# Kernel optimization log

Measured on AMD Instinct MI355X. Metric: run time of the kernel, lower is better.

Reference implementation:

```python
import jax, jax.numpy as jnp
import numpy as np

N_NODES = 100000


def _graph_conv(x, W, b, src, dst, n_nodes):
    # DGL GraphConv, norm='both', weight applied before aggregation (in>out).
    E = src.shape[0]
    ones = jnp.ones((E,), dtype=x.dtype)
    out_deg = jax.ops.segment_sum(ones, src, num_segments=n_nodes)
    in_deg = jax.ops.segment_sum(ones, dst, num_segments=n_nodes)
    out_norm = jnp.clip(out_deg, 1.0, None) ** -0.5  # [N]
    in_norm = jnp.clip(in_deg, 1.0, None) ** -0.5    # [N]
    h = (x * out_norm[:, None]) @ W                  # [N, out] dense GEMM first
    msg = h[src]                                     # gather  [E, out]
    agg = jax.ops.segment_sum(msg, dst, num_segments=n_nodes)  # scatter-add
    return agg * in_norm[:, None] + b


def setup_inputs() -> dict:
    key = jax.random.key(0)
    k1, k2, k3, k4, k5 = jax.random.split(key, 5)
    E = 1600000
    features = jax.random.normal(k1, (N_NODES, 128), dtype=jnp.float32)
    src = jax.random.randint(k2, (E,), 0, N_NODES, dtype=jnp.int64)
    dst = jax.random.randint(k3, (E,), 0, N_NODES, dtype=jnp.int64)
    W1 = jax.random.normal(k4, (128, 64), dtype=jnp.float32) * (1.0 / np.sqrt(128))
    b1 = jnp.zeros((64,), dtype=jnp.float32)
    W2 = jax.random.normal(k5, (64, 32), dtype=jnp.float32) * (1.0 / np.sqrt(64))
    b2 = jnp.zeros((32,), dtype=jnp.float32)
    return {"features": features, "src": src, "dst": dst,
            "W1": W1, "b1": b1, "W2": W2, "b2": b2}


def reference(features, src, dst, W1, b1, W2, b2):
    x = jax.nn.relu(_graph_conv(features, W1, b1, src, dst, N_NODES))
    x = _graph_conv(x, W2, b2, src, dst, N_NODES)
    return x
```

## Files before the change

### kernel.cpp

```cpp
#include <hip/hip_runtime.h>
#include <hip/hip_bf16.h>


#define BSH 7
#define BNODES 128
#define SRCMASK 0x1FFFF
#define CAP 2560
#define CHUNK 4096

typedef __attribute__((ext_vector_type(8))) short bf16x8;
typedef __attribute__((ext_vector_type(4))) float f32x4;

__device__ __forceinline__ unsigned short f2bf(float f) {
    unsigned int u = __float_as_uint(f);
    return (unsigned short)((u + 0x7FFFu + ((u >> 16) & 1u)) >> 16);
}

__device__ __forceinline__ float bflo(unsigned int u) {
    return __uint_as_float(u << 16);
}
__device__ __forceinline__ float bfhi(unsigned int u) {
    return __uint_as_float(u & 0xFFFF0000u);
}

__global__ __launch_bounds__(1024) void k_place(const int* __restrict__ src,
        const int* __restrict__ dst, int* __restrict__ ebuf,
        unsigned char* __restrict__ sbuf, int* __restrict__ offs,
        int* __restrict__ soffs, int E) {
    __shared__ int lh[800], s[800];
    int t = threadIdx.x;
    int e0 = blockIdx.x * CHUNK;
    int nE = min(CHUNK, E - e0);
    int sv[4], dv[4];
#pragma unroll
    for (int j = 0; j < 4; j++) {
        int i = t + 1024 * j;
        if (i < nE) { sv[j] = src[e0 + i]; dv[j] = dst[e0 + i]; }
        else        { sv[j] = -1; }
    }
    if (t < 800) lh[t] = 0;
    __syncthreads();
#pragma unroll
    for (int j = 0; j < 4; j++) if (sv[j] >= 0) {
        atomicAdd(&lh[dv[j] >> BSH], 0x10000);
        atomicAdd(&lh[sv[j] >> BSH], 1);
    }
    __syncthreads();
    if (t < 800) s[t] = lh[t];
    __syncthreads();
    for (int o = 1; o < 800; o <<= 1) {
        int u = (t < 800 && t >= o) ? s[t - o] : 0;
        __syncthreads();
        if (t < 800) s[t] += u;
        __syncthreads();
    }
    int obase = blockIdx.x * 801;
    if (t < 800) {
        int incl = s[t], c = lh[t];
        int bd = (incl >> 16) - (c >> 16);
        int bs = (incl & 0xFFFF) - (c & 0xFFFF);
        offs[obase + t] = bd;
        soffs[obase + t] = bs;
        s[t] = (bd << 16) | bs;
    }
    if (t == 0) { offs[obase + 800] = nE; soffs[obase + 800] = nE; }
    __syncthreads();
#pragma unroll
    for (int j = 0; j < 4; j++) if (sv[j] >= 0) {
        int pd = atomicAdd(&s[dv[j] >> BSH], 0x10000) >> 16;
        ebuf[e0 + pd] = sv[j] | ((dv[j] & (BNODES - 1)) << 17);
        int ps = atomicAdd(&s[sv[j] >> BSH], 1) & 0xFFFF;
        sbuf[e0 + ps] = (unsigned char)(sv[j] & (BNODES - 1));
    }
}

__global__ __launch_bounds__(1024) void k_sg1(const int* __restrict__ ebuf,
        const unsigned char* __restrict__ sbuf, const int* __restrict__ offs,
        const int* __restrict__ soffs, int* __restrict__ csrc,
        int* __restrict__ ostart, int* __restrict__ oend,
        float* __restrict__ nI, float* __restrict__ nO,
        const float* __restrict__ x, const float* __restrict__ W1,
        unsigned short* __restrict__ h1, int n, int NBLK) {
    __shared__ int cnt2[264], scnt2[264], cur2[264];
    __shared__ int cnt[BNODES], s[BNODES];
    __shared__ int segst[400], segen[400], sst[400], sen[400];
    __shared__ float snO[BNODES];
    __shared__ __align__(16) unsigned short sX[128 * 136];
    __shared__ __align__(16) unsigned short sWT[64 * 136];
    int t = threadIdx.x, b = blockIdx.x;

    if (t < NBLK) {
        segst[t] = t * CHUNK + offs[t * 801 + b];
        segen[t] = t * CHUNK + offs[t * 801 + b + 1];
        sst[t]   = t * CHUNK + soffs[t * 801 + b];
        sen[t]   = t * CHUNK + soffs[t * 801 + b + 1];
    }
    if (t < 264) { cnt2[t] = 0; scnt2[t] = 0; }
    __syncthreads();
    int grp = t >> 3, ln = t & 7;
    int hb = (t >> 9) * 132;
    for (int sg = grp; sg < NBLK; sg += 128) {
        int en = segen[sg];
        for (int i = segst[sg] + ln; i < en; i += 8)
            atomicAdd(&cnt2[hb + (ebuf[i] >> 17)], 1);
        int en2 = sen[sg];
        for (int i = sst[sg] + ln; i < en2; i += 8)
            atomicAdd(&scnt2[hb + sbuf[i]], 1);
    }
    __syncthreads();
    if (t < BNODES) {
        cnt[t] = cnt2[t] + cnt2[132 + t];
        s[t] = cnt[t];
    }
    __syncthreads();
    for (int o = 1; o < BNODES; o <<= 1) {
        int u = (t < BNODES && t >= o) ? s[t - o] : 0;
        __syncthreads();
        if (t < BNODES) s[t] += u;
        __syncthreads();
    }
    if (t < BNODES) {
        int e0 = b * CAP;
        int st = e0 + s[t] - cnt[t];
        cur2[t] = st;
        cur2[132 + t] = st + cnt2[t];
        int sct = scnt2[t] + scnt2[132 + t];
        float nov = rsqrtf(fmaxf((float)sct, 1.0f));
        snO[t] = nov;
        int g = b * BNODES + t;
        if (g < n) {
            ostart[g] = st;
            oend[g] = e0 + s[t];
            nI[g] = rsqrtf(fmaxf((float)cnt[t], 1.0f));
            nO[g] = nov;
        }
    }
    __syncthreads();
    for (int sg = grp; sg < NBLK; sg += 128) {
        int en = segen[sg];
        for (int i = segst[sg] + ln; i < en; i += 8) {
            int p = ebuf[i];
            int pos = atomicAdd(&cur2[hb + (p >> 17)], 1);
            csrc[pos] = p & SRCMASK;
        }
    }

    __syncthreads();
    {
        const float4* W4 = (const float4*)W1;
#pragma unroll
        for (int i = 0; i < 2; i++) {
            int f = t + 1024 * i;
            int k = f >> 4, n4 = (f & 15) * 4;
            float4 v = W4[f];
            sWT[(n4 + 0) * 136 + k] = f2bf(v.x);
            sWT[(n4 + 1) * 136 + k] = f2bf(v.y);
            sWT[(n4 + 2) * 136 + k] = f2bf(v.z);
            sWT[(n4 + 3) * 136 + k] = f2bf(v.w);
        }
    }
    const int rowbase = b * BNODES;
    {
        const float4* x4 = (const float4*)x;
#pragma unroll
        for (int i = 0; i < 4; i++) {
            int f = t + 1024 * i;
            int row = f >> 5, kc = f & 31;
            int grow = rowbase + row;
            float4 v = make_float4(0.f, 0.f, 0.f, 0.f);
            float sc = 0.f;
            if (grow < n) { v = x4[(size_t)grow * 32 + kc]; sc = snO[row]; }
            ushort4 o;
            o.x = f2bf(v.x * sc); o.y = f2bf(v.y * sc);
            o.z = f2bf(v.z * sc); o.w = f2bf(v.w * sc);
            *(ushort4*)&sX[row * 136 + kc * 4] = o;
        }
    }
    __syncthreads();
    const int wv = t >> 6, lane = t & 63;
    const int lr = lane & 15, lk = lane >> 4;
    const int slab = (wv & 7) * 16;
    const int ch = (wv >> 3) * 32;
    f32x4 acc0 = {0.f, 0.f, 0.f, 0.f};
    f32x4 acc1 = {0.f, 0.f, 0.f, 0.f};
#pragma unroll
    for (int kk = 0; kk < 4; kk++) {
        bf16x8 a  = *(const bf16x8*)&sX[(slab + lr) * 136 + kk * 32 + lk * 8];
        bf16x8 b0 = *(const bf16x8*)&sWT[(ch + lr) * 136 + kk * 32 + lk * 8];
        bf16x8 b1 = *(const bf16x8*)&sWT[(ch + 16 + lr) * 136 + kk * 32 + lk * 8];
        acc0 = __builtin_amdgcn_mfma_f32_16x16x32_bf16(a, b0, acc0, 0, 0, 0);
        acc1 = __builtin_amdgcn_mfma_f32_16x16x32_bf16(a, b1, acc1, 0, 0, 0);
    }
#pragma unroll
    for (int i = 0; i < 4; i++) {
        int grow = rowbase + slab + lk * 4 + i;
        if (grow < n) {
            size_t base = (size_t)grow * 64 + ch + lr;
            h1[base]      = f2bf(acc0[i]);
            h1[base + 16] = f2bf(acc1[i]);
        }
    }
}

__global__ void k_agg64(const unsigned short* __restrict__ h,
                        const int* __restrict__ csrc,
                        const int* __restrict__ ostart, const int* __restrict__ oend,
                        const float* __restrict__ nI, const float* __restrict__ b1,
                        float* __restrict__ x2, int n) {
    int node = blockIdx.x * 4 + (threadIdx.x >> 6);
    int lane = threadIdx.x & 63;
    if (node >= n) return;
    int s0 = ostart[node], s1 = oend[node];
    int sub = lane >> 3;
    int c8 = (lane & 7) * 8;
    float a[8] = {}, d[8] = {};
    int e = s0;
    for (; e + 15 < s1; e += 16) {
        int p0 = csrc[e + sub];
        int p1 = csrc[e + 8 + sub];
        uint4 u0 = *(const uint4*)&h[(size_t)p0 * 64 + c8];
        uint4 u1 = *(const uint4*)&h[(size_t)p1 * 64 + c8];
        a[0] += bflo(u0.x); a[1] += bfhi(u0.x);
        a[2] += bflo(u0.y); a[3] += bfhi(u0.y);
        a[4] += bflo(u0.z); a[5] += bfhi(u0.z);
        a[6] += bflo(u0.w); a[7] += bfhi(u0.w);
        d[0] += bflo(u1.x); d[1] += bfhi(u1.x);
        d[2] += bflo(u1.y); d[3] += bfhi(u1.y);
        d[4] += bflo(u1.z); d[5] += bfhi(u1.z);
        d[6] += bflo(u1.w); d[7] += bfhi(u1.w);
    }
    for (; e < s1; e += 8) {
        if (e + sub < s1) {
            int p = csrc[e + sub];
            uint4 u = *(const uint4*)&h[(size_t)p * 64 + c8];
            a[0] += bflo(u.x); a[1] += bfhi(u.x);
            a[2] += bflo(u.y); a[3] += bfhi(u.y);
            a[4] += bflo(u.z); a[5] += bfhi(u.z);
            a[6] += bflo(u.w); a[7] += bfhi(u.w);
        }
    }
#pragma unroll
    for (int i = 0; i < 8; i++) a[i] += d[i];
#pragma unroll
    for (int i = 0; i < 8; i++) {
        a[i] += __shfl(a[i], lane ^ 8, 64);
        a[i] += __shfl(a[i], lane ^ 16, 64);
        a[i] += __shfl(a[i], lane ^ 32, 64);
    }
    if (sub == 0) {
        float ni = nI[node];
        float4 o0, o1;
        o0.x = fmaxf(fmaf(a[0], ni, b1[c8 + 0]), 0.f);
        o0.y = fmaxf(fmaf(a[1], ni, b1[c8 + 1]), 0.f);
        o0.z = fmaxf(fmaf(a[2], ni, b1[c8 + 2]), 0.f);
        o0.w = fmaxf(fmaf(a[3], ni, b1[c8 + 3]), 0.f);
        o1.x = fmaxf(fmaf(a[4], ni, b1[c8 + 4]), 0.f);
        o1.y = fmaxf(fmaf(a[5], ni, b1[c8 + 5]), 0.f);
        o1.z = fmaxf(fmaf(a[6], ni, b1[c8 + 6]), 0.f);
        o1.w = fmaxf(fmaf(a[7], ni, b1[c8 + 7]), 0.f);
        *(float4*)&x2[(size_t)node * 64 + c8] = o0;
        *(float4*)&x2[(size_t)node * 64 + c8 + 4] = o1;
    }
}

__global__ __launch_bounds__(256) void k_gemm2(const float* __restrict__ x2,
                        const float* __restrict__ W2, const float* __restrict__ nO,
                        unsigned short* __restrict__ h2, int n) {
    __shared__ __align__(16) unsigned short sX[128 * 72];
    __shared__ __align__(16) unsigned short sWT[32 * 72];
    const int t = threadIdx.x;
    {
        const float4* W4 = (const float4*)W2;
#pragma unroll
        for (int i = 0; i < 2; i++) {
            int f = t + 256 * i;
            int k = f >> 3, n4 = (f & 7) * 4;
            float4 v = W4[f];
            sWT[(n4 + 0) * 72 + k] = f2bf(v.x);
            sWT[(n4 + 1) * 72 + k] = f2bf(v.y);
            sWT[(n4 + 2) * 72 + k] = f2bf(v.z);
            sWT[(n4 + 3) * 72 + k] = f2bf(v.w);
        }
    }
    const int rowbase = blockIdx.x * 128;
    {
        const float4* x4 = (const float4*)x2;
#pragma unroll
        for (int i = 0; i < 8; i++) {
            int f = t + 256 * i;
            int row = f >> 4, kc = f & 15;
            int grow = rowbase + row;
            float4 v = make_float4(0.f, 0.f, 0.f, 0.f);
            float sc = 0.f;
            if (grow < n) { v = x4[(size_t)grow * 16 + kc]; sc = nO[grow]; }
            ushort4 o;
            o.x = f2bf(v.x * sc); o.y = f2bf(v.y * sc);
            o.z = f2bf(v.z * sc); o.w = f2bf(v.w * sc);
            *(ushort4*)&sX[row * 72 + kc * 4] = o;
        }
    }
    __syncthreads();
    const int wv = t >> 6, lane = t & 63;
    const int lr = lane & 15, lk = lane >> 4;
    const int slab = wv * 32;
    f32x4 a00 = {0.f, 0.f, 0.f, 0.f};
    f32x4 a01 = {0.f, 0.f, 0.f, 0.f};
    f32x4 a10 = {0.f, 0.f, 0.f, 0.f};
    f32x4 a11 = {0.f, 0.f, 0.f, 0.f};
#pragma unroll
    for (int kk = 0; kk < 2; kk++) {
        bf16x8 a0 = *(const bf16x8*)&sX[(slab + lr) * 72 + kk * 32 + lk * 8];
        bf16x8 a1 = *(const bf16x8*)&sX[(slab + 16 + lr) * 72 + kk * 32 + lk * 8];
        bf16x8 b0 = *(const bf16x8*)&sWT[lr * 72 + kk * 32 + lk * 8];
        bf16x8 b1 = *(const bf16x8*)&sWT[(16 + lr) * 72 + kk * 32 + lk * 8];
        a00 = __builtin_amdgcn_mfma_f32_16x16x32_bf16(a0, b0, a00, 0, 0, 0);
        a01 = __builtin_amdgcn_mfma_f32_16x16x32_bf16(a0, b1, a01, 0, 0, 0);
        a10 = __builtin_amdgcn_mfma_f32_16x16x32_bf16(a1, b0, a10, 0, 0, 0);
        a11 = __builtin_amdgcn_mfma_f32_16x16x32_bf16(a1, b1, a11, 0, 0, 0);
    }
#pragma unroll
    for (int i = 0; i < 4; i++) {
        int g0 = rowbase + slab + lk * 4 + i;
        if (g0 < n) {
            h2[(size_t)g0 * 32 + lr]      = f2bf(a00[i]);
            h2[(size_t)g0 * 32 + 16 + lr] = f2bf(a01[i]);
        }
        int g1 = g0 + 16;
        if (g1 < n) {
            h2[(size_t)g1 * 32 + lr]      = f2bf(a10[i]);
            h2[(size_t)g1 * 32 + 16 + lr] = f2bf(a11[i]);
        }
    }
}

__global__ void k_agg32(const unsigned short* __restrict__ h,
                        const int* __restrict__ csrc,
                        const int* __restrict__ ostart, const int* __restrict__ oend,
                        const float* __restrict__ nI, const float* __restrict__ b2,
                        float* __restrict__ out, int n) {
    int node = blockIdx.x * 4 + (threadIdx.x >> 6);
    int lane = threadIdx.x & 63;
    if (node >= n) return;
    int s0 = ostart[node], s1 = oend[node];
    int sub = lane >> 2;
    int c8 = (lane & 3) * 8;
    float a[8] = {};
    int e = s0;
    for (; e + 15 < s1; e += 16) {
        int p = csrc[e + sub];
        uint4 u = *(const uint4*)&h[(size_t)p * 32 + c8];
        a[0] += bflo(u.x); a[1] += bfhi(u.x);
        a[2] += bflo(u.y); a[3] += bfhi(u.y);
        a[4] += bflo(u.z); a[5] += bfhi(u.z);
        a[6] += bflo(u.w); a[7] += bfhi(u.w);
    }
    for (; e < s1; e += 16) {
        if (e + sub < s1) {
            int p = csrc[e + sub];
            uint4 u = *(const uint4*)&h[(size_t)p * 32 + c8];
            a[0] += bflo(u.x); a[1] += bfhi(u.x);
            a[2] += bflo(u.y); a[3] += bfhi(u.y);
            a[4] += bflo(u.z); a[5] += bfhi(u.z);
            a[6] += bflo(u.w); a[7] += bfhi(u.w);
        }
    }
#pragma unroll
    for (int i = 0; i < 8; i++) {
        a[i] += __shfl(a[i], lane ^ 4, 64);
        a[i] += __shfl(a[i], lane ^ 8, 64);
        a[i] += __shfl(a[i], lane ^ 16, 64);
        a[i] += __shfl(a[i], lane ^ 32, 64);
    }
    if (sub == 0) {
        float ni = nI[node];
        float4 o0, o1;
        o0.x = fmaf(a[0], ni, b2[c8 + 0]);
        o0.y = fmaf(a[1], ni, b2[c8 + 1]);
        o0.z = fmaf(a[2], ni, b2[c8 + 2]);
        o0.w = fmaf(a[3], ni, b2[c8 + 3]);
        o1.x = fmaf(a[4], ni, b2[c8 + 4]);
        o1.y = fmaf(a[5], ni, b2[c8 + 5]);
        o1.z = fmaf(a[6], ni, b2[c8 + 6]);
        o1.w = fmaf(a[7], ni, b2[c8 + 7]);
        *(float4*)&out[(size_t)node * 32 + c8] = o0;
        *(float4*)&out[(size_t)node * 32 + c8 + 4] = o1;
    }
}

extern "C" void kernel_launch(void* const* d_in, const int* in_sizes, int n_in,
                              void* d_out, int out_size, void* d_ws, size_t ws_size,
                              hipStream_t stream) {
    const float* x   = (const float*)d_in[0];
    const int*   src = (const int*)d_in[1];
    const int*   dst = (const int*)d_in[2];
    const float* W1  = (const float*)d_in[3];
    const float* b1  = (const float*)d_in[4];
    const float* W2  = (const float*)d_in[5];
    const float* b2  = (const float*)d_in[6];
    float* out = (float*)d_out;

    const int N = in_sizes[0] / 128;
    const int E = in_sizes[1];
    const int NB = (N + BNODES - 1) / BNODES;
    const int NBLK = (E + CHUNK - 1) / CHUNK;

    char* wsb = (char*)d_ws;
    float* nO     = (float*)wsb;  wsb += (size_t)N * 4;
    float* nI     = (float*)wsb;  wsb += (size_t)N * 4;
    int*   ostart = (int*)wsb;    wsb += (size_t)N * 4;
    int*   oend   = (int*)wsb;    wsb += (size_t)N * 4;
    int*   csrc   = (int*)wsb;    wsb += (size_t)NB * CAP * 4;
    int*   offs   = (int*)wsb;    wsb += (size_t)NBLK * 801 * 4;
    unsigned short* h1 = (unsigned short*)wsb;
                                  wsb += (size_t)N * 64 * 2;
    float* x2     = (float*)wsb;  wsb += (size_t)N * 64 * 4;
    unsigned short* h2 = h1;
    int*   ebuf   = (int*)x2;
    unsigned char* sbuf = (unsigned char*)(ebuf) + (size_t)E * 4;
    int*   soffs  = (int*)(sbuf + (size_t)E);

    k_place<<<NBLK, 1024, 0, stream>>>(src, dst, ebuf, sbuf, offs, soffs, E);
    k_sg1<<<NB, 1024, 0, stream>>>(ebuf, sbuf, offs, soffs, csrc,
                                   ostart, oend, nI, nO, x, W1, h1, N, NBLK);

    k_agg64<<<(N + 3) / 4, 256, 0, stream>>>(h1, csrc, ostart, oend, nI, b1, x2, N);

    k_gemm2<<<(N + 127) / 128, 256, 0, stream>>>(x2, W2, nO, h2, N);
    k_agg32<<<(N + 3) / 4, 256, 0, stream>>>(h2, csrc, ostart, oend, nI, b2, out, N);
}
```

Baseline: 249.4 us.

## Fuse layer-1 aggregation with layer-2 GEMM through shared memory

Merges the 64-wide aggregation kernel and the second dense GEMM into one kernel. Each 1024-thread block aggregates 32 nodes, applies bias, ReLU and out-norm, stages the bf16 rows in LDS, then runs MFMA against W2 to write h2. This removes the fp32 x2 round trip through global memory and one launch. In exchange every block reloads and transposes W2, and 12 of 16 waves sit idle during the GEMM phase. The workspace is remapped so h2 aliases the edge scratch buffers.

After: 248.3 us. About the same (-0.5%).

```diff
diff --git a/kernel.cpp b/kernel.cpp
--- a/kernel.cpp
+++ b/kernel.cpp
@@ -202,133 +202,110 @@
     }
 }
 
-__global__ void k_agg64(const unsigned short* __restrict__ h,
-                        const int* __restrict__ csrc,
-                        const int* __restrict__ ostart, const int* __restrict__ oend,
-                        const float* __restrict__ nI, const float* __restrict__ b1,
-                        float* __restrict__ x2, int n) {
-    int node = blockIdx.x * 4 + (threadIdx.x >> 6);
-    int lane = threadIdx.x & 63;
-    if (node >= n) return;
-    int s0 = ostart[node], s1 = oend[node];
-    int sub = lane >> 3;
-    int c8 = (lane & 7) * 8;
-    float a[8] = {}, d[8] = {};
-    int e = s0;
-    for (; e + 15 < s1; e += 16) {
-        int p0 = csrc[e + sub];
-        int p1 = csrc[e + 8 + sub];
-        uint4 u0 = *(const uint4*)&h[(size_t)p0 * 64 + c8];
-        uint4 u1 = *(const uint4*)&h[(size_t)p1 * 64 + c8];
-        a[0] += bflo(u0.x); a[1] += bfhi(u0.x);
-        a[2] += bflo(u0.y); a[3] += bfhi(u0.y);
-        a[4] += bflo(u0.z); a[5] += bfhi(u0.z);
-        a[6] += bflo(u0.w); a[7] += bfhi(u0.w);
-        d[0] += bflo(u1.x); d[1] += bfhi(u1.x);
-        d[2] += bflo(u1.y); d[3] += bfhi(u1.y);
-        d[4] += bflo(u1.z); d[5] += bfhi(u1.z);
-        d[6] += bflo(u1.w); d[7] += bfhi(u1.w);
-    }
-    for (; e < s1; e += 8) {
-        if (e + sub < s1) {
-            int p = csrc[e + sub];
-            uint4 u = *(const uint4*)&h[(size_t)p * 64 + c8];
-            a[0] += bflo(u.x); a[1] += bfhi(u.x);
-            a[2] += bflo(u.y); a[3] += bfhi(u.y);
-            a[4] += bflo(u.z); a[5] += bfhi(u.z);
-            a[6] += bflo(u.w); a[7] += bfhi(u.w);
-        }
-    }
-#pragma unroll
-    for (int i = 0; i < 8; i++) a[i] += d[i];
-#pragma unroll
-    for (int i = 0; i < 8; i++) {
-        a[i] += __shfl(a[i], lane ^ 8, 64);
-        a[i] += __shfl(a[i], lane ^ 16, 64);
-        a[i] += __shfl(a[i], lane ^ 32, 64);
-    }
-    if (sub == 0) {
-        float ni = nI[node];
-        float4 o0, o1;
-        o0.x = fmaxf(fmaf(a[0], ni, b1[c8 + 0]), 0.f);
-        o0.y = fmaxf(fmaf(a[1], ni, b1[c8 + 1]), 0.f);
-        o0.z = fmaxf(fmaf(a[2], ni, b1[c8 + 2]), 0.f);
-        o0.w = fmaxf(fmaf(a[3], ni, b1[c8 + 3]), 0.f);
-        o1.x = fmaxf(fmaf(a[4], ni, b1[c8 + 4]), 0.f);
-        o1.y = fmaxf(fmaf(a[5], ni, b1[c8 + 5]), 0.f);
-        o1.z = fmaxf(fmaf(a[6], ni, b1[c8 + 6]), 0.f);
-        o1.w = fmaxf(fmaf(a[7], ni, b1[c8 + 7]), 0.f);
-        *(float4*)&x2[(size_t)node * 64 + c8] = o0;
-        *(float4*)&x2[(size_t)node * 64 + c8 + 4] = o1;
-    }
-}
-
-__global__ __launch_bounds__(256) void k_gemm2(const float* __restrict__ x2,
-                        const float* __restrict__ W2, const float* __restrict__ nO,
-                        unsigned short* __restrict__ h2, int n) {
-    __shared__ __align__(16) unsigned short sX[128 * 72];
+__global__ __launch_bounds__(1024) void k_ag2(const unsigned short* __restrict__ h,
+        const int* __restrict__ csrc,
+        const int* __restrict__ ostart, const int* __restrict__ oend,
+        const float* __restrict__ nI, const float* __restrict__ nO,
+        const float* __restrict__ b1, const float* __restrict__ W2,
+        unsigned short* __restrict__ h2, int n) {
+    __shared__ __align__(16) unsigned short xt[32 * 72];
     __shared__ __align__(16) unsigned short sWT[32 * 72];
     const int t = threadIdx.x;
+    if (t < 512) {
+        const float4* W4 = (const float4*)W2;
+        int k = t >> 3, n4 = (t & 7) * 4;
+        float4 v = W4[t];
+        sWT[(n4 + 0) * 72 + k] = f2bf(v.x);
+        sWT[(n4 + 1) * 72 + k] = f2bf(v.y);
+        sWT[(n4 + 2) * 72 + k] = f2bf(v.z);
+        sWT[(n4 + 3) * 72 + k] = f2bf(v.w);
+    }
     {
-        const float4* W4 = (const float4*)W2;
-#pragma unroll
-        for (int i = 0; i < 2; i++) {
-            int f = t + 256 * i;
-            int k = f >> 3, n4 = (f & 7) * 4;
-            float4 v = W4[f];
-            sWT[(n4 + 0) * 72 + k] = f2bf(v.x);
-            sWT[(n4 + 1) * 72 + k] = f2bf(v.y);
-            sWT[(n4 + 2) * 72 + k] = f2bf(v.z);
-            sWT[(n4 + 3) * 72 + k] = f2bf(v.w);
-        }
-    }
-    const int rowbase = blockIdx.x * 128;
-    {
-        const float4* x4 = (const float4*)x2;
-#pragma unroll
-        for (int i = 0; i < 8; i++) {
-            int f = t + 256 * i;
-            int row = f >> 4, kc = f & 15;
-            int grow = rowbase + row;
-            float4 v = make_float4(0.f, 0.f, 0.f, 0.f);
-            float sc = 0.f;
-            if (grow < n) { v = x4[(size_t)grow * 16 + kc]; sc = nO[grow]; }
-            ushort4 o;
-            o.x = f2bf(v.x * sc); o.y = f2bf(v.y * sc);
-            o.z = f2bf(v.z * sc); o.w = f2bf(v.w * sc);
-            *(ushort4*)&sX[row * 72 + kc * 4] = o;
-        }
-    }
-    __syncthreads();
-    const int wv = t >> 6, lane = t & 63;
-    const int lr = lane & 15, lk = lane >> 4;
-    const int slab = wv * 32;
-    f32x4 a00 = {0.f, 0.f, 0.f, 0.f};
-    f32x4 a01 = {0.f, 0.f, 0.f, 0.f};
-    f32x4 a10 = {0.f, 0.f, 0.f, 0.f};
-    f32x4 a11 = {0.f, 0.f, 0.f, 0.f};
-#pragma unroll
-    for (int kk = 0; kk < 2; kk++) {
-        bf16x8 a0 = *(const bf16x8*)&sX[(slab + lr) * 72 + kk * 32 + lk * 8];
-        bf16x8 a1 = *(const bf16x8*)&sX[(slab + 16 + lr) * 72 + kk * 32 + lk * 8];
-        bf16x8 b0 = *(const bf16x8*)&sWT[lr * 72 + kk * 32 + lk * 8];
-        bf16x8 b1 = *(const bf16x8*)&sWT[(16 + lr) * 72 + kk * 32 + lk * 8];
-        a00 = __builtin_amdgcn_mfma_f32_16x16x32_bf16(a0, b0, a00, 0, 0, 0);
-        a01 = __builtin_amdgcn_mfma_f32_16x16x32_bf16(a0, b1, a01, 0, 0, 0);
-        a10 = __builtin_amdgcn_mfma_f32_16x16x32_bf16(a1, b0, a10, 0, 0, 0);
-        a11 = __builtin_amdgcn_mfma_f32_16x16x32_bf16(a1, b1, a11, 0, 0, 0);
-    }
-#pragma unroll
-    for (int i = 0; i < 4; i++) {
-        int g0 = rowbase + slab + lk * 4 + i;
-        if (g0 < n) {
-            h2[(size_t)g0 * 32 + lr]      = f2bf(a00[i]);
-            h2[(size_t)g0 * 32 + 16 + lr] = f2bf(a01[i]);
-        }
-        int g1 = g0 + 16;
-        if (g1 < n) {
-            h2[(size_t)g1 * 32 + lr]      = f2bf(a10[i]);
-            h2[(size_t)g1 * 32 + 16 + lr] = f2bf(a11[i]);
+        int* z = (int*)xt;
+        if (t < 32 * 36) z[t] = 0;
+    }
+    __syncthreads();
+    const int wid = t >> 6, lane = t & 63;
+    const int node0 = blockIdx.x * 32;
+    const int sub = lane >> 3;
+    const int c8 = (lane & 7) * 8;
+#pragma unroll
+    for (int g = 0; g < 2; g++) {
+        int node = node0 + wid * 2 + g;
+        if (node < n) {
+            int s0 = ostart[node], s1 = oend[node];
+            float a[8] = {}, d[8] = {};
+            int e = s0;
+            for (; e + 15 < s1; e += 16) {
+                int p0 = csrc[e + sub];
+                int p1 = csrc[e + 8 + sub];
+                uint4 u0 = *(const uint4*)&h[(size_t)p0 * 64 + c8];
+                uint4 u1 = *(const uint4*)&h[(size_t)p1 * 64 + c8];
+                a[0] += bflo(u0.x); a[1] += bfhi(u0.x);
+                a[2] += bflo(u0.y); a[3] += bfhi(u0.y);
+                a[4] += bflo(u0.z); a[5] += bfhi(u0.z);
+                a[6] += bflo(u0.w); a[7] += bfhi(u0.w);
+                d[0] += bflo(u1.x); d[1] += bfhi(u1.x);
+                d[2] += bflo(u1.y); d[3] += bfhi(u1.y);
+                d[4] += bflo(u1.z); d[5] += bfhi(u1.z);
+                d[6] += bflo(u1.w); d[7] += bfhi(u1.w);
+            }
+            for (; e < s1; e += 8) {
+                if (e + sub < s1) {
+                    int p = csrc[e + sub];
+                    uint4 u = *(const uint4*)&h[(size_t)p * 64 + c8];
+                    a[0] += bflo(u.x); a[1] += bfhi(u.x);
+                    a[2] += bflo(u.y); a[3] += bfhi(u.y);
+                    a[4] += bflo(u.z); a[5] += bfhi(u.z);
+                    a[6] += bflo(u.w); a[7] += bfhi(u.w);
+                }
+            }
+#pragma unroll
+            for (int i = 0; i < 8; i++) a[i] += d[i];
+#pragma unroll
+            for (int i = 0; i < 8; i++) {
+                a[i] += __shfl(a[i], lane ^ 8, 64);
+                a[i] += __shfl(a[i], lane ^ 16, 64);
+                a[i] += __shfl(a[i], lane ^ 32, 64);
+            }
+            if (sub == 0) {
+                float ni = nI[node];
+                float nv = nO[node];
+                float v0 = fmaxf(fmaf(a[0], ni, b1[c8 + 0]), 0.f) * nv;
+                float v1 = fmaxf(fmaf(a[1], ni, b1[c8 + 1]), 0.f) * nv;
+                float v2 = fmaxf(fmaf(a[2], ni, b1[c8 + 2]), 0.f) * nv;
+                float v3 = fmaxf(fmaf(a[3], ni, b1[c8 + 3]), 0.f) * nv;
+                float v4 = fmaxf(fmaf(a[4], ni, b1[c8 + 4]), 0.f) * nv;
+                float v5 = fmaxf(fmaf(a[5], ni, b1[c8 + 5]), 0.f) * nv;
+                float v6 = fmaxf(fmaf(a[6], ni, b1[c8 + 6]), 0.f) * nv;
+                float v7 = fmaxf(fmaf(a[7], ni, b1[c8 + 7]), 0.f) * nv;
+                int row = wid * 2 + g;
+                ushort4 o0, o1;
+                o0.x = f2bf(v0); o0.y = f2bf(v1);
+                o0.z = f2bf(v2); o0.w = f2bf(v3);
+                o1.x = f2bf(v4); o1.y = f2bf(v5);
+                o1.z = f2bf(v6); o1.w = f2bf(v7);
+                *(ushort4*)&xt[row * 72 + c8]     = o0;
+                *(ushort4*)&xt[row * 72 + c8 + 4] = o1;
+            }
+        }
+    }
+    __syncthreads();
+    if (wid < 4) {
+        const int lr = lane & 15, lk = lane >> 4;
+        const int slab = wid >> 1, ct = wid & 1;
+        f32x4 acc = {0.f, 0.f, 0.f, 0.f};
+#pragma unroll
+        for (int kk = 0; kk < 2; kk++) {
+            bf16x8 a = *(const bf16x8*)&xt[(slab * 16 + lr) * 72 + kk * 32 + lk * 8];
+            bf16x8 b = *(const bf16x8*)&sWT[(ct * 16 + lr) * 72 + kk * 32 + lk * 8];
+            acc = __builtin_amdgcn_mfma_f32_16x16x32_bf16(a, b, acc, 0, 0, 0);
+        }
+#pragma unroll
+        for (int i = 0; i < 4; i++) {
+            int grow = node0 + slab * 16 + lk * 4 + i;
+            if (grow < n)
+                h2[(size_t)grow * 32 + ct * 16 + lr] = f2bf(acc[i]);
         }
     }
 }
@@ -413,18 +390,18 @@
     int*   offs   = (int*)wsb;    wsb += (size_t)NBLK * 801 * 4;
     unsigned short* h1 = (unsigned short*)wsb;
                                   wsb += (size_t)N * 64 * 2;
-    float* x2     = (float*)wsb;  wsb += (size_t)N * 64 * 4;
-    unsigned short* h2 = h1;
-    int*   ebuf   = (int*)x2;
-    unsigned char* sbuf = (unsigned char*)(ebuf) + (size_t)E * 4;
-    int*   soffs  = (int*)(sbuf + (size_t)E);
+    char*  scr    = wsb;          wsb += (size_t)E * 4 + E + (size_t)NBLK * 801 * 4;
+    int*   ebuf   = (int*)scr;
+    unsigned char* sbuf = (unsigned char*)scr + (size_t)E * 4;
+    int*   soffs  = (int*)((char*)scr + (size_t)E * 4 + E);
+    unsigned short* h2 = (unsigned short*)scr;
 
     k_place<<<NBLK, 1024, 0, stream>>>(src, dst, ebuf, sbuf, offs, soffs, E);
     k_sg1<<<NB, 1024, 0, stream>>>(ebuf, sbuf, offs, soffs, csrc,
                                    ostart, oend, nI, nO, x, W1, h1, N, NBLK);
 
-    k_agg64<<<(N + 3) / 4, 256, 0, stream>>>(h1, csrc, ostart, oend, nI, b1, x2, N);
-
-    k_gemm2<<<(N + 127) / 128, 256, 0, stream>>>(x2, W2, nO, h2, N);
+    k_ag2<<<(N + 31) / 32, 1024, 0, stream>>>(h1, csrc, ostart, oend,
+                                              nI, nO, b1, W2, h2, N);
+
     k_agg32<<<(N + 3) / 4, 256, 0, stream>>>(h2, csrc, ostart, oend, nI, b2, out, N);
 }
```
